# Optimization experiments

Hardware: AMD Instinct MI355X
Metric: run time of the kernel (lower is better)

The kernel has to match this reference:

```python
import jax, jax.numpy as jnp
import numpy as np

N = 2097152
N_LAYERS = 32
N_SUB = 8


def setup_inputs() -> dict:
    key = jax.random.key(0)
    k1, k2, k3, k4 = jax.random.split(key, 4)
    return {
        "x": jax.random.normal(k1, (N, 2), dtype=jnp.float32),
        "act_w": 0.05 * jax.random.normal(k2, (N_LAYERS,), dtype=jnp.float32),
        "bias_b": 0.05 * jax.random.normal(k3, (N_LAYERS, 2), dtype=jnp.float32),
        "lin_w": 0.05 * jax.random.normal(k4, (N_LAYERS, N_SUB), dtype=jnp.float32),
    }


def _forward_chain(q, p, act_w, bias_b, lin_w):
    # Apply Modules[0..end] with inverse=0.
    n_layers, n_sub = lin_w.shape
    for i in range(n_layers):
        # activation module: up adds w*tanh(p) to q, low adds w*tanh(q) to p
        if i % 2 == 0:
            q = q + act_w[i] * jnp.tanh(p)
        else:
            p = p + act_w[i] * jnp.tanh(q)
        # bias module (inserted at j == 0)
        q = q + bias_b[i, 0]
        p = p + bias_b[i, 1]
        # linear shear modules
        for j in range(n_sub):
            if j % 2 == 0:   # linear_module_up: q += w*p
                q = q + lin_w[i, j] * p
            else:            # linear_module_low: p += w*q
                p = p + lin_w[i, j] * q
    return q, p


def _inverse_chain(q, p, act_w, bias_b, lin_w):
    # Apply all modules in reverse order with inverse=1 (negated weights).
    n_layers, n_sub = lin_w.shape
    for i in reversed(range(n_layers)):
        for j in reversed(range(n_sub)):
            if j % 2 == 0:
                q = q - lin_w[i, j] * p
            else:
                p = p - lin_w[i, j] * q
        q = q - bias_b[i, 0]
        p = p - bias_b[i, 1]
        if i % 2 == 0:
            q = q - act_w[i] * jnp.tanh(p)
        else:
            p = p - act_w[i] * jnp.tanh(q)
    return q, p


def reference(x, act_w, bias_b, lin_w):
    q, p = x[..., 0], x[..., 1]
    q, p = _forward_chain(q, p, act_w, bias_b, lin_w)
    # time reversal: multiply by [1, -1]
    p = -p
    q, p = _inverse_chain(q, p, act_w, bias_b, lin_w)
    # final module-0 inverse is included in _inverse_chain; scale by [1, -1]
    return jnp.stack([q, -p], axis=-1)
```

## Files before the change

### kernel.cpp

```cpp
#include <hip/hip_runtime.h>

constexpr int NL = 32;
constexpr int PPT = 8;

__device__ __forceinline__ float tanh_poly(float x) {
#if __has_builtin(__builtin_amdgcn_fmed3f)
    float t = __builtin_amdgcn_fmed3f(x, -3.4f, 3.4f);
#else
    float t = fminf(fmaxf(x, -3.4f), 3.4f);
#endif
    float s = t * t;
    float u = fmaf(s, 2.3524e-06f, -1.000059e-04f);
    u = fmaf(s, u, 1.7302740e-03f);
    u = fmaf(s, u, -1.5874717e-02f);
    u = fmaf(s, u, 8.5976700e-02f);
    u = fmaf(s, u, -3.0595090e-01f);
    u = fmaf(s, u, 9.9691910e-01f);
    return t * u;
}

__global__ __launch_bounds__(256, 4) void sympnet_main(
    const float* __restrict__ x,
    const float* __restrict__ act_w,
    const float* __restrict__ bias_b,
    const float* __restrict__ lin_w,
    float* __restrict__ out,
    int nthreads)
{
    __shared__ float4 tf[NL][2];
    __shared__ float4 ti[NL][2];

    int t = threadIdx.x;
    if (t < NL) {
        float m00 = 1.f, m01 = 0.f, m10 = 0.f, m11 = 1.f;
        #pragma unroll
        for (int j = 0; j < 8; ++j) {
            float w = lin_w[t * 8 + j];
            if ((j & 1) == 0) { m00 = fmaf(w, m10, m00); m01 = fmaf(w, m11, m01); }
            else              { m10 = fmaf(w, m00, m10); m11 = fmaf(w, m01, m11); }
        }
        float b0 = bias_b[2 * t], b1 = bias_b[2 * t + 1], aw = act_w[t];
        tf[t][0] = make_float4(m00, m01, m10, m11);
        tf[t][1] = make_float4(fmaf(m00, b0, m01 * b1), fmaf(m10, b0, m11 * b1), aw, 0.f);
        float s = (t == NL - 1) ? -1.f : 1.f;
        ti[t][0] = make_float4(m11, s * (-m01), -m10, s * m00);
        ti[t][1] = make_float4(-b0, -b1, -aw, 0.f);
    }
    __syncthreads();

    int gid = blockIdx.x * blockDim.x + t;
    const float2* x2 = (const float2*)x;
    float2* o2 = (float2*)out;

    float Q[PPT], P[PPT];
    #pragma unroll
    for (int k = 0; k < PPT; ++k) {
        float2 v = x2[gid + k * nthreads];
        Q[k] = v.x; P[k] = v.y;
    }

    #pragma unroll 1
    for (int i = 0; i < NL; i += 2) {
        float4 Fm = tf[i][0],     Fc = tf[i][1];
        float4 Gm = tf[i + 1][0], Gc = tf[i + 1][1];
        #pragma unroll
        for (int k = 0; k < PPT; ++k) {
            float Qa = fmaf(Fc.z, tanh_poly(P[k]), Q[k]);
            float Qn = fmaf(Fm.x, Qa, fmaf(Fm.y, P[k], Fc.x));
            float Pn = fmaf(Fm.z, Qa, fmaf(Fm.w, P[k], Fc.y));
            float Pa = fmaf(Gc.z, tanh_poly(Qn), Pn);
            Q[k] = fmaf(Gm.x, Qn, fmaf(Gm.y, Pa, Gc.x));
            P[k] = fmaf(Gm.z, Qn, fmaf(Gm.w, Pa, Gc.y));
        }
    }


    #pragma unroll 1
    for (int i = NL - 1; i > 0; i -= 2) {
        float4 Gm = ti[i][0],     Gc = ti[i][1];
        float4 Fm = ti[i - 1][0], Fc = ti[i - 1][1];
        #pragma unroll
        for (int k = 0; k < PPT; ++k) {
            float Qn = fmaf(Gm.x, Q[k], fmaf(Gm.y, P[k], Gc.x));
            float Pn = fmaf(Gm.z, Q[k], fmaf(Gm.w, P[k], Gc.y));
            Pn = fmaf(Gc.z, tanh_poly(Qn), Pn);
            float Q2 = fmaf(Fm.x, Qn, fmaf(Fm.y, Pn, Fc.x));
            float P2 = fmaf(Fm.z, Qn, fmaf(Fm.w, Pn, Fc.y));
            Q[k] = fmaf(Fc.z, tanh_poly(P2), Q2);
            P[k] = P2;
        }
    }

    #pragma unroll
    for (int k = 0; k < PPT; ++k) {
        float2 o; o.x = Q[k]; o.y = -P[k];
        o2[gid + k * nthreads] = o;
    }
}

extern "C" void kernel_launch(void* const* d_in, const int* in_sizes, int n_in,
                              void* d_out, int out_size, void* d_ws, size_t ws_size,
                              hipStream_t stream) {
    const float* x      = (const float*)d_in[0];
    const float* act_w  = (const float*)d_in[1];
    const float* bias_b = (const float*)d_in[2];
    const float* lin_w  = (const float*)d_in[3];
    float* out = (float*)d_out;

    int npts = in_sizes[0] / 2;
    int nthreads = npts / PPT;
    int blocks = nthreads / 256;
    sympnet_main<<<blocks, 256, 0, stream>>>(x, act_w, bias_b, lin_w, out, nthreads);
}
```

Measured before the change: 106.9 us.

## Precompute layer tables in a separate kernel and read them from global memory with prefetch

Moves the per-layer matrix and bias table construction into a small one-block kernel that writes to workspace, so the main kernel no longer rebuilds tables in LDS and calls __syncthreads. The main kernel loads table entries from global memory (uniform, likely scalar loads) and prefetches the next layer pair's entries one iteration ahead. Points per thread drop from 8 to 4 with contiguous float4 loads and stores. The tanh polynomial is re-evaluated in Estrin form to shorten the dependency chain. The costs are an extra kernel launch, less independent work per thread to hide latency, and twice as many blocks.

```diff
diff --git a/kernel.cpp b/kernel.cpp
--- a/kernel.cpp
+++ b/kernel.cpp
@@ -1,101 +1,115 @@
 #include <hip/hip_runtime.h>
 
-constexpr int NL = 32;
-constexpr int PPT = 8;
+constexpr int PPT = 4;
 
-__device__ __forceinline__ float tanh_poly(float x) {
+__device__ __forceinline__ float tanh_est(float x) {
 #if __has_builtin(__builtin_amdgcn_fmed3f)
     float t = __builtin_amdgcn_fmed3f(x, -3.4f, 3.4f);
 #else
     float t = fminf(fmaxf(x, -3.4f), 3.4f);
 #endif
-    float s = t * t;
-    float u = fmaf(s, 2.3524e-06f, -1.000059e-04f);
-    u = fmaf(s, u, 1.7302740e-03f);
-    u = fmaf(s, u, -1.5874717e-02f);
-    u = fmaf(s, u, 8.5976700e-02f);
-    u = fmaf(s, u, -3.0595090e-01f);
-    u = fmaf(s, u, 9.9691910e-01f);
-    return t * u;
+    float s  = t * t;
+    float s2 = s * s;
+    float s4 = s2 * s2;
+    float e0 = fmaf(s, -3.0595090e-01f, 9.9691910e-01f);
+    float e1 = fmaf(s, -1.5874717e-02f, 8.5976700e-02f);
+    float e2 = fmaf(s, -1.000059e-04f, 1.7302740e-03f);
+    float g0 = fmaf(s2, e1, e0);
+    float g1 = fmaf(s2, 2.3524e-06f, e2);
+    return t * fmaf(s4, g1, g0);
+}
+
+__global__ void build_tables(const float* __restrict__ act_w,
+                             const float* __restrict__ bias_b,
+                             const float* __restrict__ lin_w,
+                             float4* __restrict__ tab)
+{
+    int t = threadIdx.x;
+    if (t >= 32) return;
+    float m00 = 1.f, m01 = 0.f, m10 = 0.f, m11 = 1.f;
+    #pragma unroll
+    for (int j = 0; j < 8; ++j) {
+        float w = lin_w[t * 8 + j];
+        if ((j & 1) == 0) { m00 = fmaf(w, m10, m00); m01 = fmaf(w, m11, m01); }
+        else              { m10 = fmaf(w, m00, m10); m11 = fmaf(w, m01, m11); }
+    }
+    float b0 = bias_b[2 * t], b1 = bias_b[2 * t + 1], aw = act_w[t];
+    float C0 = fmaf(m00, b0, m01 * b1);
+    float C1 = fmaf(m10, b0, m11 * b1);
+    if ((t & 1) == 0) {
+        tab[(t >> 1) * 4 + 0] = make_float4(m00, m01, m10, m11);
+        tab[(t >> 1) * 4 + 1] = make_float4(C0, C1, aw, 0.f);
+        int it = (30 - t) >> 1;
+        tab[64 + it * 4 + 2] = make_float4(m11, -m01, -m10, m00);
+        tab[64 + it * 4 + 3] = make_float4(-b0, -b1, -aw, 0.f);
+    } else {
+        tab[(t >> 1) * 4 + 2] = make_float4(m00, m01, m10, m11);
+        tab[(t >> 1) * 4 + 3] = make_float4(C0, C1, aw, 0.f);
+        int it = (31 - t) >> 1;
+        float s = (t == 31) ? -1.f : 1.f;
+        tab[64 + it * 4 + 0] = make_float4(m11, s * (-m01), -m10, s * m00);
+        tab[64 + it * 4 + 1] = make_float4(-b0, -b1, -aw, 0.f);
+    }
 }
 
 __global__ __launch_bounds__(256, 4) void sympnet_main(
     const float* __restrict__ x,
-    const float* __restrict__ act_w,
-    const float* __restrict__ bias_b,
-    const float* __restrict__ lin_w,
-    float* __restrict__ out,
-    int nthreads)
+    const float4* __restrict__ tab,
+    float* __restrict__ out)
 {
-    __shared__ float4 tf[NL][2];
-    __shared__ float4 ti[NL][2];
-
-    int t = threadIdx.x;
-    if (t < NL) {
-        float m00 = 1.f, m01 = 0.f, m10 = 0.f, m11 = 1.f;
-        #pragma unroll
-        for (int j = 0; j < 8; ++j) {
-            float w = lin_w[t * 8 + j];
-            if ((j & 1) == 0) { m00 = fmaf(w, m10, m00); m01 = fmaf(w, m11, m01); }
-            else              { m10 = fmaf(w, m00, m10); m11 = fmaf(w, m01, m11); }
-        }
-        float b0 = bias_b[2 * t], b1 = bias_b[2 * t + 1], aw = act_w[t];
-        tf[t][0] = make_float4(m00, m01, m10, m11);
-        tf[t][1] = make_float4(fmaf(m00, b0, m01 * b1), fmaf(m10, b0, m11 * b1), aw, 0.f);
-        float s = (t == NL - 1) ? -1.f : 1.f;
-        ti[t][0] = make_float4(m11, s * (-m01), -m10, s * m00);
-        ti[t][1] = make_float4(-b0, -b1, -aw, 0.f);
-    }
-    __syncthreads();
-
-    int gid = blockIdx.x * blockDim.x + t;
-    const float2* x2 = (const float2*)x;
-    float2* o2 = (float2*)out;
+    int gid = blockIdx.x * blockDim.x + threadIdx.x;
+    const float4* x4 = (const float4*)x;
+    float4* out4 = (float4*)out;
+    long base = (long)gid * 2;
 
     float Q[PPT], P[PPT];
-    #pragma unroll
-    for (int k = 0; k < PPT; ++k) {
-        float2 v = x2[gid + k * nthreads];
-        Q[k] = v.x; P[k] = v.y;
+    {
+        float4 v0 = x4[base], v1 = x4[base + 1];
+        Q[0] = v0.x; P[0] = v0.y; Q[1] = v0.z; P[1] = v0.w;
+        Q[2] = v1.x; P[2] = v1.y; Q[3] = v1.z; P[3] = v1.w;
     }
 
+    float4 Fm = tab[0], Fc = tab[1], Gm = tab[2], Gc = tab[3];
     #pragma unroll 1
-    for (int i = 0; i < NL; i += 2) {
-        float4 Fm = tf[i][0],     Fc = tf[i][1];
-        float4 Gm = tf[i + 1][0], Gc = tf[i + 1][1];
+    for (int it = 0; it < 16; ++it) {
+        const float4* np = tab + (it + 1) * 4;
+        float4 nFm = np[0], nFc = np[1], nGm = np[2], nGc = np[3];
         #pragma unroll
         for (int k = 0; k < PPT; ++k) {
-            float Qa = fmaf(Fc.z, tanh_poly(P[k]), Q[k]);
+            float Qa = fmaf(Fc.z, tanh_est(P[k]), Q[k]);
             float Qn = fmaf(Fm.x, Qa, fmaf(Fm.y, P[k], Fc.x));
             float Pn = fmaf(Fm.z, Qa, fmaf(Fm.w, P[k], Fc.y));
-            float Pa = fmaf(Gc.z, tanh_poly(Qn), Pn);
+            float Pa = fmaf(Gc.z, tanh_est(Qn), Pn);
             Q[k] = fmaf(Gm.x, Qn, fmaf(Gm.y, Pa, Gc.x));
             P[k] = fmaf(Gm.z, Qn, fmaf(Gm.w, Pa, Gc.y));
         }
+        Fm = nFm; Fc = nFc; Gm = nGm; Gc = nGc;
     }
 
 
+    float4 Am = Fm, Ac = Fc, Bm = Gm, Bc = Gc;
     #pragma unroll 1
-    for (int i = NL - 1; i > 0; i -= 2) {
-        float4 Gm = ti[i][0],     Gc = ti[i][1];
-        float4 Fm = ti[i - 1][0], Fc = ti[i - 1][1];
+    for (int it = 0; it < 16; ++it) {
+        int nx = 64 + ((it < 15) ? (it + 1) : it) * 4;
+        const float4* np = tab + nx;
+        float4 nAm = np[0], nAc = np[1], nBm = np[2], nBc = np[3];
         #pragma unroll
         for (int k = 0; k < PPT; ++k) {
-            float Qn = fmaf(Gm.x, Q[k], fmaf(Gm.y, P[k], Gc.x));
-            float Pn = fmaf(Gm.z, Q[k], fmaf(Gm.w, P[k], Gc.y));
-            Pn = fmaf(Gc.z, tanh_poly(Qn), Pn);
-            float Q2 = fmaf(Fm.x, Qn, fmaf(Fm.y, Pn, Fc.x));
-            float P2 = fmaf(Fm.z, Qn, fmaf(Fm.w, Pn, Fc.y));
-            Q[k] = fmaf(Fc.z, tanh_poly(P2), Q2);
+            float Qn = fmaf(Am.x, Q[k], fmaf(Am.y, P[k], Ac.x));
+            float Pn = fmaf(Am.z, Q[k], fmaf(Am.w, P[k], Ac.y));
+            Pn = fmaf(Ac.z, tanh_est(Qn), Pn);
+            float Q2 = fmaf(Bm.x, Qn, fmaf(Bm.y, Pn, Bc.x));
+            float P2 = fmaf(Bm.z, Qn, fmaf(Bm.w, Pn, Bc.y));
+            Q[k] = fmaf(Bc.z, tanh_est(P2), Q2);
             P[k] = P2;
         }
+        Am = nAm; Ac = nAc; Bm = nBm; Bc = nBc;
     }
 
-    #pragma unroll
-    for (int k = 0; k < PPT; ++k) {
-        float2 o; o.x = Q[k]; o.y = -P[k];
-        o2[gid + k * nthreads] = o;
-    }
+    float4 o0 = make_float4(Q[0], -P[0], Q[1], -P[1]);
+    float4 o1 = make_float4(Q[2], -P[2], Q[3], -P[3]);
+    out4[base] = o0;
+    out4[base + 1] = o1;
 }
 
 extern "C" void kernel_launch(void* const* d_in, const int* in_sizes, int n_in,
@@ -106,9 +120,12 @@
     const float* bias_b = (const float*)d_in[2];
     const float* lin_w  = (const float*)d_in[3];
     float* out = (float*)d_out;
+    float4* tab = (float4*)d_ws;
+
+    build_tables<<<1, 64, 0, stream>>>(act_w, bias_b, lin_w, tab);
 
     int npts = in_sizes[0] / 2;
     int nthreads = npts / PPT;
     int blocks = nthreads / 256;
-    sympnet_main<<<blocks, 256, 0, stream>>>(x, act_w, bias_b, lin_w, out, nthreads);
+    sympnet_main<<<blocks, 256, 0, stream>>>(x, tab, out);
 }
```

New measurement: 107.0 us. About the same (+0.1%).
